# Performance work log

Measured on AMD Instinct MI355X. Metric: run time of the kernel, lower is better.

The kernel has to match this reference:

```python
import jax, jax.numpy as jnp
import numpy as np
import math

N, E, R = 50000, 800000, 32
DIN = 128
H, D = 8, 16          # num_heads, head_dim; H*D == out_ent_feats == 128
HOP = 5
ALPHA = 0.1
EPS = 1e-5


def layer_norm(x, g, b):
    m = jnp.mean(x, axis=-1, keepdims=True)
    v = jnp.mean((x - m) ** 2, axis=-1, keepdims=True)
    return (x - m) * jax.lax.rsqrt(v + EPS) * g + b


def segment_softmax(e, dst, num_nodes):
    # e: [E, H] scores, softmax over incoming edges of each dst node
    m = jax.ops.segment_max(e, dst, num_segments=num_nodes)      # [N, H]
    ex = jnp.exp(e - m[dst])
    s = jax.ops.segment_sum(ex, dst, num_segments=num_nodes)     # [N, H]
    return ex / s[dst]


def setup_inputs() -> dict:
    key = jax.random.key(0)
    ks = jax.random.split(key, 12)
    gain = 0.02  # small init scale (small_init_gain-style)
    ent_feat = jax.random.normal(ks[0], (N, DIN), dtype=jnp.float32)
    rel_feat = jax.random.normal(ks[1], (R, DIN), dtype=jnp.float32)
    src = jax.random.randint(ks[2], (E,), 0, N, dtype=jnp.int32)
    # guarantee every node has in-degree >= 1 (DGL raises otherwise)
    dst_rand = jax.random.randint(ks[3], (E - N,), 0, N, dtype=jnp.int32)
    dst = jnp.concatenate([jnp.arange(N, dtype=jnp.int32), dst_rand])
    rid = jax.random.randint(ks[4], (E,), 0, R, dtype=jnp.int32)
    W_head = jax.random.normal(ks[5], (DIN, H * D), dtype=jnp.float32) * gain
    W_tail = jax.random.normal(ks[6], (DIN, H * D), dtype=jnp.float32) * gain
    W_ent = jax.random.normal(ks[7], (DIN, H * D), dtype=jnp.float32) * gain
    W_rel = jax.random.normal(ks[8], (DIN, H * D), dtype=jnp.float32) * gain
    attn_r = jax.random.normal(ks[9], (1, H, D), dtype=jnp.float32) * gain
    W1 = jax.random.normal(ks[10], (H * D, 4 * H * D), dtype=jnp.float32) * gain
    W2 = jax.random.normal(ks[11], (4 * H * D, H * D), dtype=jnp.float32) * gain
    return dict(
        ent_feat=ent_feat, rel_feat=rel_feat, src=src, dst=dst, rid=rid,
        W_head=W_head, W_tail=W_tail, W_ent=W_ent, W_rel=W_rel, attn_r=attn_r,
        ln_ent_g=jnp.ones((DIN,), jnp.float32), ln_ent_b=jnp.zeros((DIN,), jnp.float32),
        ln_rel_g=jnp.ones((DIN,), jnp.float32), ln_rel_b=jnp.zeros((DIN,), jnp.float32),
        ff_ln_g=jnp.ones((H * D,), jnp.float32), ff_ln_b=jnp.zeros((H * D,), jnp.float32),
        W1=W1, b1=jnp.zeros((4 * H * D,), jnp.float32),
        W2=W2, b2=jnp.zeros((H * D,), jnp.float32),
    )


def _forward(ent_feat, rel_feat, src, dst, rid,
             W_head, W_tail, W_ent, W_rel, attn_r,
             ln_ent_g, ln_ent_b, ln_rel_g, ln_rel_b, ff_ln_g, ff_ln_b,
             W1, b1, W2, b2):
    n = ent_feat.shape[0]
    x = layer_norm(ent_feat, ln_ent_g, ln_ent_b)
    feat_head = (x @ W_head).reshape(n, H, D)
    feat_tail = (x @ W_tail).reshape(n, H, D)
    feat_ent = (x @ W_ent).reshape(n, H, D)

    # per-edge dot-product attention score: u_dot_v('eh','et')
    e = jnp.sum(feat_head[src] * feat_tail[dst], axis=-1)          # [E, H]

    r = layer_norm(rel_feat, ln_rel_g, ln_rel_b)
    feat_rel = (r @ W_rel).reshape(R, H, D)
    er = jnp.sum(feat_rel * attn_r, axis=-1)                       # [R, H]
    e = e * er[rid]                                                # [E, H]

    # e_mul_v with log_in = log(in_degree) of dst node
    deg = jax.ops.segment_sum(jnp.ones((e.shape[0],), e.dtype), dst, num_segments=n)
    log_in = jnp.log(jnp.maximum(deg, 1.0))                        # [N]
    e = e * log_in[dst][:, None] / math.sqrt(D)

    a = segment_softmax(e, dst, n)                                 # [E, H]

    # PPR diffusion: feat <- (1-alpha) * A^T feat + alpha * feat_0
    feat = feat_ent
    for _ in range(HOP):
        msg = feat[src] * a[:, :, None]                            # [E, H, D]
        agg = jax.ops.segment_sum(msg, dst, num_segments=n)        # [N, H, D]
        feat = (1.0 - ALPHA) * agg + ALPHA * feat_ent

    # residual (Identity: in_ent_feats == out_ent_feats)
    rst = feat + ent_feat.reshape(n, H, D)
    rst = rst.reshape(n, H * D)

    h = layer_norm(rst, ff_ln_g, ff_ln_b)
    ff = jax.nn.relu(h @ W1 + b1) @ W2 + b2
    return ff + rst


def reference(ent_feat, rel_feat, src, dst, rid,
              W_head, W_tail, W_ent, W_rel, attn_r,
              ln_ent_g, ln_ent_b, ln_rel_g, ln_rel_b, ff_ln_g, ff_ln_b,
              W1, b1, W2, b2):
    return _forward(ent_feat, rel_feat, src, dst, rid,
                    W_head, W_tail, W_ent, W_rel, attn_r,
                    ln_ent_g, ln_ent_b, ln_rel_g, ln_rel_b, ff_ln_g, ff_ln_b,
                    W1, b1, W2, b2)
```

## Files before the change

kernel.cpp:

```cpp
#include <hip/hip_runtime.h>
#include <hip/hip_bf16.h>

#define N_NODES 50000
#define N_EDGES 800000
#define N_REL 32
#define DIN 128
#define NH 8
#define HD 16
#define FF_HID 512
#define EPS_LN 1e-5f
#define NBUCK 8
#define BDIV 6250
#define BCAP 114688

typedef __attribute__((ext_vector_type(8))) short bf16x8;
typedef __attribute__((ext_vector_type(4))) float f32x4;
typedef __attribute__((ext_vector_type(2))) float f32x2;
typedef unsigned short ushort_t;
typedef unsigned int uint_t;

static __device__ __forceinline__ unsigned short f2bf(float f) {
    union { float f; unsigned u; } v; v.f = f;
    unsigned r = (v.u + 0x7fffu + ((v.u >> 16) & 1u)) >> 16;
    return (unsigned short)r;
}
static __device__ __forceinline__ float bf2f(unsigned u16) {
    union { unsigned u; float f; } v; v.u = u16 << 16; return v.f;
}
static __device__ __forceinline__ unsigned char f2fp8(float f) {
    return (unsigned char)(__builtin_amdgcn_cvt_pk_fp8_f32(f, f, 0, false) & 0xff);
}
static __device__ __forceinline__ uint_t f2fp8x2(float x0, float x1) {
    return (__builtin_amdgcn_cvt_pk_fp8_f32(x0, x1, 0, false) & 0xffffu);
}
static __device__ __forceinline__ void fp8x4_to_f32(uint_t w, float* o) {
    f32x2 lo = __builtin_amdgcn_cvt_pk_f32_fp8(w, false);
    f32x2 hi = __builtin_amdgcn_cvt_pk_f32_fp8(w, true);
    o[0] = lo.x; o[1] = lo.y; o[2] = hi.x; o[3] = hi.y;
}

static __device__ __forceinline__ void pack_dev(const float* __restrict__ W,
                                                short* __restrict__ out, int K, int Ncols,
                                                int idx) {
    int KT = K >> 5;
    int l = idx & 63;
    int tile = idx >> 6;
    int kt = tile & (KT - 1);
    int ct = tile / KT;
    int c = ct * 16 + (l & 15);
    int k0 = kt * 32 + ((l >> 4) * 8);
    bf16x8 v;
#pragma unroll
    for (int j = 0; j < 8; j++) v[j] = (short)f2bf(W[(size_t)(k0 + j) * Ncols + c]);
    *(bf16x8*)(out + (size_t)idx * 8) = v;
}

#define C0_BIN 512
__global__ __launch_bounds__(256) void combo0_kernel(
    const int* __restrict__ src, const int* __restrict__ dst, const int* __restrict__ rid,
    int* __restrict__ gcnt, int* __restrict__ bdst, int* __restrict__ bpay,
    const float* __restrict__ W1, short* __restrict__ W1p, const float* __restrict__ W2,
    short* __restrict__ W2p, const float* __restrict__ Wh, short* __restrict__ Whp,
    const float* __restrict__ Wt, short* __restrict__ Wtp, const float* __restrict__ We,
    short* __restrict__ Wep, const float* __restrict__ rel_feat,
    const float* __restrict__ gr, const float* __restrict__ br,
    const float* __restrict__ W_rel, const float* __restrict__ attn_r,
    float* __restrict__ er) {
    __shared__ float red[128];
    __shared__ float xsr[128];
    __shared__ float prod[128];
    __shared__ int cnt[NBUCK];
    __shared__ int sbase[NBUCK];
    int b = blockIdx.x, tid = threadIdx.x;
    if (b < C0_BIN) {
        const int chunk = (N_EDGES + C0_BIN - 1) / C0_BIN;
        int i0 = b * chunk;
        int i1 = min(i0 + chunk, N_EDGES);
        int rounds = (i1 - i0 + 255) >> 8;
        for (int r = 0; r < rounds; r++) {
            int i = i0 + (r << 8) + tid;
            if (tid < NBUCK) cnt[tid] = 0;
            __syncthreads();
            int d = 0, b8 = 0, rank = 0, py = 0;
            bool v = i < i1;
            if (v) {
                d = dst[i];
                b8 = d / BDIV;
                py = src[i] | (rid[i] << 16);
                rank = atomicAdd(&cnt[b8], 1);
            }
            __syncthreads();
            if (tid < NBUCK) sbase[tid] = atomicAdd(&gcnt[tid], cnt[tid]);
            __syncthreads();
            if (v) {
                size_t pos = (size_t)b8 * BCAP + sbase[b8] + rank;
                bdst[pos] = d;
                bpay[pos] = py;
            }
            __syncthreads();
        }
    } else if (b < C0_BIN + 32) {
        pack_dev(W1, W1p, DIN, FF_HID, (b - C0_BIN) * 256 + tid);
    } else if (b < C0_BIN + 64) {
        pack_dev(W2, W2p, FF_HID, DIN, (b - C0_BIN - 32) * 256 + tid);
    } else if (b < C0_BIN + 72) {
        pack_dev(Wh, Whp, DIN, DIN, (b - C0_BIN - 64) * 256 + tid);
    } else if (b < C0_BIN + 80) {
        pack_dev(Wt, Wtp, DIN, DIN, (b - C0_BIN - 72) * 256 + tid);
    } else if (b < C0_BIN + 88) {
        pack_dev(We, Wep, DIN, DIN, (b - C0_BIN - 80) * 256 + tid);
    } else {
        int r = b - (C0_BIN + 88);
        float x = 0.f;
        if (tid < 128) {
            x = rel_feat[r * DIN + tid];
            red[tid] = x;
        }
        __syncthreads();
        for (int off = 64; off > 0; off >>= 1) {
            if (tid < off) red[tid] += red[tid + off];
            __syncthreads();
        }
        float mean = red[0] * (1.f / DIN);
        __syncthreads();
        if (tid < 128) red[tid] = x * x;
        __syncthreads();
        for (int off = 64; off > 0; off >>= 1) {
            if (tid < off) red[tid] += red[tid + off];
            __syncthreads();
        }
        float var = red[0] * (1.f / DIN) - mean * mean;
        float rs = rsqrtf(var + EPS_LN);
        if (tid < 128) xsr[tid] = (x - mean) * rs * gr[tid] + br[tid];
        __syncthreads();
        if (tid < 128) {
            float acc = 0.f;
            for (int k = 0; k < DIN; k++) acc += xsr[k] * W_rel[k * DIN + tid];
            prod[tid] = acc * attn_r[tid];
        }
        __syncthreads();
        if (tid < NH) {
            float s = 0.f;
            for (int d = 0; d < HD; d++) s += prod[tid * HD + d];
            er[r * NH + tid] = s;
        }
    }
}

#define NHB 8
__global__ __launch_bounds__(256) void hist2_kernel(const int* __restrict__ bdst,
                                                    const int* __restrict__ gcnt,
                                                    int* __restrict__ deg) {
    __shared__ int lhist[BDIV];
    int blk = blockIdx.x, tid = threadIdx.x;
    int b8 = blk & 7, sub = blk >> 3;
    for (int i = tid; i < BDIV; i += 256) lhist[i] = 0;
    __syncthreads();
    int cnt = gcnt[b8];
    int chunk = (cnt + NHB - 1) / NHB;
    int i0 = sub * chunk;
    int i1 = min(i0 + chunk, cnt);
    const int* bp = bdst + (size_t)b8 * BCAP;
    int w0 = b8 * BDIV;
    for (int i = i0 + tid; i < i1; i += 256) atomicAdd(&lhist[bp[i] - w0], 1);
    __syncthreads();
    for (int i = tid; i < BDIV; i += 256) {
        int v = lhist[i];
        if (v) atomicAdd(&deg[w0 + i], v);
    }
}

#define NS_SCAN 196
__global__ __launch_bounds__(256) void combo_mid_kernel(
    const int* __restrict__ deg, int* __restrict__ row_off,
    const float* __restrict__ ent, const float* __restrict__ g, const float* __restrict__ b,
    const short* __restrict__ Whp, const short* __restrict__ Wtp,
    const short* __restrict__ Wep, unsigned char* __restrict__ hent,
    ushort_t* __restrict__ tail_bf) {
    __shared__ float xs[32][128];
    __shared__ short hsb[32][136];
    int blk = blockIdx.x, tid = threadIdx.x;
    if (blk < NS_SCAN) {
        __shared__ int lscan[256];
        __shared__ int ws4[4];
        int n = N_NODES;
        int start = blk * 256;
        int partial = 0;
        for (int i = tid; i < start; i += 256) partial += deg[i];
        for (int m = 32; m > 0; m >>= 1) partial += __shfl_down(partial, m);
        int wid = tid >> 6, lane = tid & 63;
        if (lane == 0) ws4[wid] = partial;
        __syncthreads();
        int sbase = ws4[0] + ws4[1] + ws4[2] + ws4[3];
        int i = start + tid;
        int v = (i < n) ? deg[i] : 0;
        lscan[tid] = v;
        __syncthreads();
        for (int off = 1; off < 256; off <<= 1) {
            int t = (tid >= off) ? lscan[tid - off] : 0;
            __syncthreads();
            lscan[tid] += t;
            __syncthreads();
        }
        if (i < n) row_off[i] = sbase + lscan[tid] - v;
        if (i == n - 1) row_off[n] = sbase + lscan[tid];
        return;
    }
    int base = (blk - NS_SCAN) * 32;
    {
        int c = tid & 127, rb = tid >> 7;
#pragma unroll
        for (int j = 0; j < 16; j++) {
            int r = j * 2 + rb;
            int row = base + r;
            xs[r][c] = (row < N_NODES) ? ent[(size_t)row * DIN + c] : 0.f;
        }
    }
    __syncthreads();
    int wave = tid >> 6, lane = tid & 63;
    {
        float g0 = g[lane], g1 = g[lane + 64], bb0 = b[lane], bb1 = b[lane + 64];
        for (int r = wave * 8; r < wave * 8 + 8; r++) {
            float x0 = xs[r][lane], x1 = xs[r][lane + 64];
            float s1 = x0 + x1, s2 = x0 * x0 + x1 * x1;
            for (int m = 1; m < 64; m <<= 1) {
                s1 += __shfl_xor(s1, m);
                s2 += __shfl_xor(s2, m);
            }
            float mean = s1 * (1.f / DIN);
            float var = s2 * (1.f / DIN) - mean * mean;
            float rs = rsqrtf(var + EPS_LN);
            hsb[r][lane] = (short)f2bf((x0 - mean) * rs * g0 + bb0);
            hsb[r][lane + 64] = (short)f2bf((x1 - mean) * rs * g1 + bb1);
        }
    }
    __syncthreads();
    bf16x8 a[2][4];
#pragma unroll
    for (int rt = 0; rt < 2; rt++)
#pragma unroll
        for (int kt = 0; kt < 4; kt++)
            a[rt][kt] = *(const bf16x8*)&hsb[rt * 16 + (lane & 15)][kt * 32 + (lane >> 4) * 8];
#pragma unroll
    for (int m = 0; m < 3; m++) {
        const bf16x8* bp = (m == 0)   ? (const bf16x8*)Whp
                           : (m == 1) ? (const bf16x8*)Wtp
                                      : (const bf16x8*)Wep;
#pragma unroll
        for (int c2 = 0; c2 < 2; c2++) {
            int ct = wave * 2 + c2;
            f32x4 acc0 = {0.f, 0.f, 0.f, 0.f}, acc1 = {0.f, 0.f, 0.f, 0.f};
#pragma unroll
            for (int kt = 0; kt < 4; kt++) {
                bf16x8 bf = bp[(ct * 4 + kt) * 64 + lane];
                acc0 = __builtin_amdgcn_mfma_f32_16x16x32_bf16(a[0][kt], bf, acc0, 0, 0, 0);
                acc1 = __builtin_amdgcn_mfma_f32_16x16x32_bf16(a[1][kt], bf, acc1, 0, 0, 0);
            }
            int col = ct * 16 + (lane & 15);
            int h = col >> 4, k = col & 15;
            int r0 = (lane >> 4) * 4;
#pragma unroll
            for (int j = 0; j < 4; j++) {
                int row0 = base + r0 + j, row1 = base + 16 + r0 + j;
                if (m == 0) {
                    if (row0 < N_NODES) hent[(size_t)row0 * 256 + h * 32 + k] = f2fp8(acc0[j]);
                    if (row1 < N_NODES) hent[(size_t)row1 * 256 + h * 32 + k] = f2fp8(acc1[j]);
                } else if (m == 1) {
                    if (row0 < N_NODES) tail_bf[(size_t)row0 * DIN + col] = f2bf(acc0[j]);
                    if (row1 < N_NODES) tail_bf[(size_t)row1 * DIN + col] = f2bf(acc1[j]);
                } else {
                    if (row0 < N_NODES)
                        hent[(size_t)row0 * 256 + h * 32 + 16 + k] = f2fp8(acc0[j]);
                    if (row1 < N_NODES)
                        hent[(size_t)row1 * 256 + h * 32 + 16 + k] = f2fp8(acc1[j]);
                }
            }
        }
    }
}

__global__ __launch_bounds__(256) void scatter_kernel(
    const int* __restrict__ bdst, const int* __restrict__ bpay,
    const int* __restrict__ gcnt, const int* __restrict__ row_off,
    int* __restrict__ cursor, int* __restrict__ sr_perm) {
    int blk = blockIdx.x, tid = threadIdx.x;
    int b8 = blk & 7, sub = blk >> 3;
    int cnt = gcnt[b8];
    int chunk = (cnt + 127) >> 7;
    int i0 = sub * chunk;
    int i1 = min(i0 + chunk, cnt);
    const int* bd = bdst + (size_t)b8 * BCAP;
    const int* bpp = bpay + (size_t)b8 * BCAP;
    for (int i = i0 + tid; i < i1; i += 256) {
        int d = bd[i];
        int p = row_off[d] + atomicAdd(&cursor[d], 1);
        sr_perm[p] = bpp[i];
    }
}

__global__ __launch_bounds__(256) void score_hop_kernel(
    const unsigned char* __restrict__ hent, const ushort_t* __restrict__ tail_bf,
    const float* __restrict__ er, const int* __restrict__ row_off,
    const int* __restrict__ sr_perm, ushort_t* __restrict__ a_bf,
    float* __restrict__ inv9, unsigned char* __restrict__ fout) {
    int wid = threadIdx.x >> 6;
    int u = blockIdx.x * 4 + wid;
    int lane = threadIdx.x & 63;
    int h = lane & 7, esub = lane >> 3;
    int p0 = row_off[u], p1 = row_off[u + 1];
    int deg = p1 - p0;
    float scale = logf((float)(deg > 0 ? deg : 1)) * 0.25f;
    float t[16];
    {
        const uint_t* tp = (const uint_t*)(tail_bf + (size_t)u * DIN + h * HD);
#pragma unroll
        for (int i = 0; i < 8; i++) {
            uint_t w = tp[i];
            t[2 * i] = bf2f(w & 0xffffu);
            t[2 * i + 1] = bf2f(w >> 16);
        }
    }
    float ssum = 0.f;
    float acc[16];
#pragma unroll
    for (int k = 0; k < 16; k++) acc[k] = 0.f;
    for (int p = p0 + esub; p < p1; p += 8) {
        int v = sr_perm[p];
        int s = v & 0xffff;
        int rr = v >> 16;
        const uint4* hp = (const uint4*)(hent + (size_t)s * 256 + h * 32);
        uint4 hw = hp[0];
        uint4 ew = hp[1];
        float hv[16], ev[16];
        fp8x4_to_f32(hw.x, hv + 0); fp8x4_to_f32(hw.y, hv + 4);
        fp8x4_to_f32(hw.z, hv + 8); fp8x4_to_f32(hw.w, hv + 12);
        fp8x4_to_f32(ew.x, ev + 0); fp8x4_to_f32(ew.y, ev + 4);
        fp8x4_to_f32(ew.z, ev + 8); fp8x4_to_f32(ew.w, ev + 12);
        float dot = 0.f;
#pragma unroll
        for (int k = 0; k < 16; k++) dot += t[k] * hv[k];
        float e = dot * er[rr * NH + h] * scale;
        float sx = expf(e);
        a_bf[(size_t)p * NH + h] = f2bf(sx);
        ssum += sx;
#pragma unroll
        for (int k = 0; k < 16; k++) acc[k] += sx * ev[k];
    }
    ssum += __shfl_xor(ssum, 8);
    ssum += __shfl_xor(ssum, 16);
    ssum += __shfl_xor(ssum, 32);
#pragma unroll
    for (int k = 0; k < 16; k++) {
        acc[k] += __shfl_xor(acc[k], 8);
        acc[k] += __shfl_xor(acc[k], 16);
        acc[k] += __shfl_xor(acc[k], 32);
    }
    if (esub == 0) {
        float iv = 0.9f / ssum;
        inv9[(size_t)u * NH + h] = iv;
        const uint4 eu = *(const uint4*)(hent + (size_t)u * 256 + h * 32 + 16);
        float e0[16];
        fp8x4_to_f32(eu.x, e0 + 0); fp8x4_to_f32(eu.y, e0 + 4);
        fp8x4_to_f32(eu.z, e0 + 8); fp8x4_to_f32(eu.w, e0 + 12);
        float x[16];
#pragma unroll
        for (int k = 0; k < 16; k++) x[k] = iv * acc[k] + 0.1f * e0[k];
        uint4 ov;
        ov.x = f2fp8x2(x[0], x[1]) | (f2fp8x2(x[2], x[3]) << 16);
        ov.y = f2fp8x2(x[4], x[5]) | (f2fp8x2(x[6], x[7]) << 16);
        ov.z = f2fp8x2(x[8], x[9]) | (f2fp8x2(x[10], x[11]) << 16);
        ov.w = f2fp8x2(x[12], x[13]) | (f2fp8x2(x[14], x[15]) << 16);
        *(uint4*)(fout + (size_t)u * DIN + h * HD) = ov;
    }
}

template <bool OUT_BF>
__global__ __launch_bounds__(256) void diffuse8_kernel(
    const unsigned char* __restrict__ fin8, const unsigned char* __restrict__ hent,
    const ushort_t* __restrict__ a_bf, const int* __restrict__ sr_perm,
    const int* __restrict__ row_off, const float* __restrict__ inv9,
    void* __restrict__ fout) {
    int wid = threadIdx.x >> 6;
    int u = blockIdx.x * 4 + wid;
    int lane = threadIdx.x & 63;
    int c = lane & 7;
    int g = lane >> 3;
    int p0 = row_off[u], p1 = row_off[u + 1];
    float acc[16];
#pragma unroll
    for (int j = 0; j < 16; j++) acc[j] = 0.f;
    for (int p = p0; p < p1; p += 8) {
        int pe = p + g;
        bool valid = pe < p1;
        int pc = valid ? pe : (p1 - 1);
        int s = sr_perm[pc] & 0xffff;
        float a = valid ? bf2f(a_bf[(size_t)pc * NH + c]) : 0.f;
        uint4 w = *(const uint4*)(fin8 + (size_t)s * DIN + 16 * c);
        float v[16];
        fp8x4_to_f32(w.x, v + 0);
        fp8x4_to_f32(w.y, v + 4);
        fp8x4_to_f32(w.z, v + 8);
        fp8x4_to_f32(w.w, v + 12);
#pragma unroll
        for (int j = 0; j < 16; j++) acc[j] += a * v[j];
    }
#pragma unroll
    for (int j = 0; j < 16; j++) {
        acc[j] += __shfl_xor(acc[j], 8);
        acc[j] += __shfl_xor(acc[j], 16);
        acc[j] += __shfl_xor(acc[j], 32);
    }
    if (g == 0) {
        float iv = inv9[(size_t)u * NH + c];
        uint4 ew = *(const uint4*)(hent + (size_t)u * 256 + c * 32 + 16);
        float e0[16];
        fp8x4_to_f32(ew.x, e0 + 0);
        fp8x4_to_f32(ew.y, e0 + 4);
        fp8x4_to_f32(ew.z, e0 + 8);
        fp8x4_to_f32(ew.w, e0 + 12);
        float x[16];
#pragma unroll
        for (int j = 0; j < 16; j++) x[j] = iv * acc[j] + 0.1f * e0[j];
        size_t o = (size_t)u * DIN + 16 * c;
        if (OUT_BF) {
            uint4 ov0, ov1;
            ov0.x = (uint_t)f2bf(x[0]) | ((uint_t)f2bf(x[1]) << 16);
            ov0.y = (uint_t)f2bf(x[2]) | ((uint_t)f2bf(x[3]) << 16);
            ov0.z = (uint_t)f2bf(x[4]) | ((uint_t)f2bf(x[5]) << 16);
            ov0.w = (uint_t)f2bf(x[6]) | ((uint_t)f2bf(x[7]) << 16);
            ov1.x = (uint_t)f2bf(x[8]) | ((uint_t)f2bf(x[9]) << 16);
            ov1.y = (uint_t)f2bf(x[10]) | ((uint_t)f2bf(x[11]) << 16);
            ov1.z = (uint_t)f2bf(x[12]) | ((uint_t)f2bf(x[13]) << 16);
            ov1.w = (uint_t)f2bf(x[14]) | ((uint_t)f2bf(x[15]) << 16);
            *(uint4*)((ushort_t*)fout + o) = ov0;
            *(uint4*)((ushort_t*)fout + o + 8) = ov1;
        } else {
            uint4 ov;
            ov.x = f2fp8x2(x[0], x[1]) | (f2fp8x2(x[2], x[3]) << 16);
            ov.y = f2fp8x2(x[4], x[5]) | (f2fp8x2(x[6], x[7]) << 16);
            ov.z = f2fp8x2(x[8], x[9]) | (f2fp8x2(x[10], x[11]) << 16);
            ov.w = f2fp8x2(x[12], x[13]) | (f2fp8x2(x[14], x[15]) << 16);
            *(uint4*)((unsigned char*)fout + o) = ov;
        }
    }
}

static __device__ __forceinline__ int hid_idx(int row, int col) {
    return row * 512 + ((((col >> 3) & 63) ^ (row & 7)) << 3) + (col & 7);
}
__global__ __launch_bounds__(256) void ffn_mfma_kernel(
    const ushort_t* __restrict__ feat, const float* __restrict__ ent0,
    const float* __restrict__ g, const float* __restrict__ b,
    const short* __restrict__ W1p, const float* __restrict__ b1,
    const short* __restrict__ W2p, const float* __restrict__ b2,
    float* __restrict__ out) {
    __shared__ ushort_t rst_bf[16][136];
    __shared__ short hs[16][136];
    __shared__ short hid[16 * 512];
    int tid = threadIdx.x;
    int base = blockIdx.x * 16;
    int wave = tid >> 6, lane = tid & 63;
    {
        int c = tid & 127, rb = tid >> 7;
#pragma unroll
        for (int j = 0; j < 8; j++) {
            int r = j * 2 + rb;
            int row = base + r;
            float v = 0.f;
            if (row < N_NODES) {
                size_t idx = (size_t)row * DIN + c;
                v = bf2f(feat[idx]) + ent0[idx];
            }
            rst_bf[r][c] = f2bf(v);
        }
    }
    __syncthreads();
    {
        float g0 = g[lane], g1 = g[lane + 64], bb0 = b[lane], bb1 = b[lane + 64];
        for (int r = wave * 4; r < wave * 4 + 4; r++) {
            float x0 = bf2f(rst_bf[r][lane]), x1 = bf2f(rst_bf[r][lane + 64]);
            float s1 = x0 + x1, s2 = x0 * x0 + x1 * x1;
            for (int m = 1; m < 64; m <<= 1) {
                s1 += __shfl_xor(s1, m);
                s2 += __shfl_xor(s2, m);
            }
            float mean = s1 * (1.f / DIN);
            float var = s2 * (1.f / DIN) - mean * mean;
            float rs = rsqrtf(var + EPS_LN);
            hs[r][lane] = (short)f2bf((x0 - mean) * rs * g0 + bb0);
            hs[r][lane + 64] = (short)f2bf((x1 - mean) * rs * g1 + bb1);
        }
    }
    __syncthreads();
    {
        bf16x8 a[4];
#pragma unroll
        for (int kt = 0; kt < 4; kt++)
            a[kt] = *(const bf16x8*)&hs[lane & 15][kt * 32 + (lane >> 4) * 8];
        const bf16x8* bp = (const bf16x8*)W1p;
        for (int cti = 0; cti < 8; cti++) {
            int ct = wave * 8 + cti;
            f32x4 acc0 = {0.f, 0.f, 0.f, 0.f};
#pragma unroll
            for (int kt = 0; kt < 4; kt++) {
                bf16x8 bf = bp[(ct * 4 + kt) * 64 + lane];
                acc0 = __builtin_amdgcn_mfma_f32_16x16x32_bf16(a[kt], bf, acc0, 0, 0, 0);
            }
            int col = ct * 16 + (lane & 15);
            float bv = b1[col];
            int r0 = (lane >> 4) * 4;
#pragma unroll
            for (int j = 0; j < 4; j++)
                hid[hid_idx(r0 + j, col)] = (short)f2bf(fmaxf(acc0[j] + bv, 0.f));
        }
    }
    __syncthreads();
    {
        f32x4 acc[2] = {{0.f, 0.f, 0.f, 0.f}, {0.f, 0.f, 0.f, 0.f}};
        const bf16x8* bp2 = (const bf16x8*)W2p;
        for (int kt = 0; kt < 16; kt++) {
            int col8 = kt * 32 + (lane >> 4) * 8;
            bf16x8 a0 = *(const bf16x8*)&hid[hid_idx(lane & 15, col8)];
#pragma unroll
            for (int c2 = 0; c2 < 2; c2++) {
                int ct = wave * 2 + c2;
                bf16x8 bf = bp2[(ct * 16 + kt) * 64 + lane];
                acc[c2] = __builtin_amdgcn_mfma_f32_16x16x32_bf16(a0, bf, acc[c2], 0, 0, 0);
            }
        }
#pragma unroll
        for (int c2 = 0; c2 < 2; c2++) {
            int col = (wave * 2 + c2) * 16 + (lane & 15);
            float bv = b2[col];
            int r0 = (lane >> 4) * 4;
#pragma unroll
            for (int j = 0; j < 4; j++) {
                int row = base + r0 + j;
                if (row < N_NODES)
                    out[(size_t)row * DIN + col] = acc[c2][j] + bv + bf2f(rst_bf[r0 + j][col]);
            }
        }
    }
}

extern "C" void kernel_launch(void* const* d_in, const int* in_sizes, int n_in,
                              void* d_out, int out_size, void* d_ws, size_t ws_size,
                              hipStream_t stream) {
    const float* ent_feat = (const float*)d_in[0];
    const float* rel_feat = (const float*)d_in[1];
    const int* src = (const int*)d_in[2];
    const int* dst = (const int*)d_in[3];
    const int* rid = (const int*)d_in[4];
    const float* W_head = (const float*)d_in[5];
    const float* W_tail = (const float*)d_in[6];
    const float* W_ent = (const float*)d_in[7];
    const float* W_rel = (const float*)d_in[8];
    const float* attn_r = (const float*)d_in[9];
    const float* ln_ent_g = (const float*)d_in[10];
    const float* ln_ent_b = (const float*)d_in[11];
    const float* ln_rel_g = (const float*)d_in[12];
    const float* ln_rel_b = (const float*)d_in[13];
    const float* ff_ln_g = (const float*)d_in[14];
    const float* ff_ln_b = (const float*)d_in[15];
    const float* W1 = (const float*)d_in[16];
    const float* b1 = (const float*)d_in[17];
    const float* W2 = (const float*)d_in[18];
    const float* b2 = (const float*)d_in[19];
    float* out = (float*)d_out;

    const int N = N_NODES, E = N_EDGES;

    char* cur = (char*)d_ws;
    auto alloc = [&](size_t bytes, size_t align) -> void* {
        uintptr_t p = (uintptr_t)cur;
        p = (p + align - 1) & ~(uintptr_t)(align - 1);
        cur = (char*)(p + bytes);
        return (void*)p;
    };
    ushort_t* tail_bf = (ushort_t*)alloc((size_t)N * DIN * 2, 16);
    unsigned char* hent = (unsigned char*)alloc((size_t)N * 256, 16);
    unsigned char* f8A = (unsigned char*)alloc((size_t)N * DIN, 16);
    unsigned char* f8B = (unsigned char*)alloc((size_t)N * DIN, 16);
    int* bdst = (int*)alloc((size_t)NBUCK * BCAP * 4, 16);
    int* bpay = (int*)alloc((size_t)NBUCK * BCAP * 4, 16);
    int* sr_perm = (int*)alloc((size_t)E * 4, 16);
    int* row_off = (int*)alloc((size_t)(N + 1) * 4, 16);
    int* deg = (int*)alloc(((size_t)2 * N + NBUCK) * 4, 16);
    int* cursor = deg + N;
    int* gcnt = deg + 2 * N;
    float* er = (float*)alloc((size_t)N_REL * NH * 4, 16);
    float* inv9 = (float*)alloc((size_t)N * NH * 4, 16);
    short* W1p = (short*)alloc((size_t)DIN * FF_HID * 2, 16);
    short* W2p = (short*)alloc((size_t)FF_HID * DIN * 2, 16);
    short* Whp = (short*)alloc((size_t)DIN * DIN * 2, 16);
    short* Wtp = (short*)alloc((size_t)DIN * DIN * 2, 16);
    short* Wep = (short*)alloc((size_t)DIN * DIN * 2, 16);
    ushort_t* a_fit = (ushort_t*)alloc((size_t)E * NH * 2, 16);
    bool a_in_ws = ((size_t)(cur - (char*)d_ws) <= ws_size);
    ushort_t* a_bf = a_in_ws ? a_fit : (ushort_t*)d_out;

    hipMemsetAsync(deg, 0, sizeof(int) * ((size_t)2 * N + NBUCK), stream);
    combo0_kernel<<<632, 256, 0, stream>>>(src, dst, rid, gcnt, bdst, bpay, W1, W1p, W2,
                                           W2p, W_head, Whp, W_tail, Wtp, W_ent, Wep,
                                           rel_feat, ln_rel_g, ln_rel_b, W_rel, attn_r,
                                           er);
    hist2_kernel<<<NBUCK * NHB, 256, 0, stream>>>(bdst, gcnt, deg);
    int nblk32 = (N + 31) / 32;
    combo_mid_kernel<<<NS_SCAN + nblk32, 256, 0, stream>>>(
        deg, row_off, ent_feat, ln_ent_g, ln_ent_b, Whp, Wtp, Wep, hent, tail_bf);
    scatter_kernel<<<1024, 256, 0, stream>>>(bdst, bpay, gcnt, row_off, cursor, sr_perm);
    score_hop_kernel<<<N / 4, 256, 0, stream>>>(hent, tail_bf, er, row_off, sr_perm,
                                                a_bf, inv9, f8A);
    diffuse8_kernel<false><<<N / 4, 256, 0, stream>>>(f8A, hent, a_bf, sr_perm, row_off,
                                                      inv9, f8B);
    diffuse8_kernel<false><<<N / 4, 256, 0, stream>>>(f8B, hent, a_bf, sr_perm, row_off,
                                                      inv9, f8A);
    diffuse8_kernel<false><<<N / 4, 256, 0, stream>>>(f8A, hent, a_bf, sr_perm, row_off,
                                                      inv9, f8B);
    diffuse8_kernel<true><<<N / 4, 256, 0, stream>>>(f8B, hent, a_bf, sr_perm, row_off,
                                                     inv9, tail_bf);
    int nblk16 = (N + 15) / 16;
    ffn_mfma_kernel<<<nblk16, 256, 0, stream>>>(tail_bf, ent_feat, ff_ln_g, ff_ln_b, W1p,
                                                b1, W2p, b2, out);
}
```

Before: 353.2 us.

## Fuse histogram with projection GEMM kernel and software-prefetch edge indices in gather loops

The degree histogram now runs in the same launch as the entity layernorm/projection blocks, and the prefix scan moves into its own small kernel. This overlaps histogram work with the GEMM instead of the scan overlapping with the GEMM. Separately, the score and diffusion loops load the next edge's index and attention weight one iteration ahead, so the dependent gather latency is partly hidden. The cost is a different kernel count and a bit more register pressure from the prefetch.

Result: slower. 362.2 us (+2.6%).

```diff
diff --git a/kernel.cpp b/kernel.cpp
--- a/kernel.cpp
+++ b/kernel.cpp
@@ -147,66 +147,38 @@
     }
 }
 
+#define C_HP_HIST 64
 #define NHB 8
-__global__ __launch_bounds__(256) void hist2_kernel(const int* __restrict__ bdst,
-                                                    const int* __restrict__ gcnt,
-                                                    int* __restrict__ deg) {
-    __shared__ int lhist[BDIV];
-    int blk = blockIdx.x, tid = threadIdx.x;
-    int b8 = blk & 7, sub = blk >> 3;
-    for (int i = tid; i < BDIV; i += 256) lhist[i] = 0;
-    __syncthreads();
-    int cnt = gcnt[b8];
-    int chunk = (cnt + NHB - 1) / NHB;
-    int i0 = sub * chunk;
-    int i1 = min(i0 + chunk, cnt);
-    const int* bp = bdst + (size_t)b8 * BCAP;
-    int w0 = b8 * BDIV;
-    for (int i = i0 + tid; i < i1; i += 256) atomicAdd(&lhist[bp[i] - w0], 1);
-    __syncthreads();
-    for (int i = tid; i < BDIV; i += 256) {
-        int v = lhist[i];
-        if (v) atomicAdd(&deg[w0 + i], v);
-    }
-}
-
-#define NS_SCAN 196
-__global__ __launch_bounds__(256) void combo_mid_kernel(
-    const int* __restrict__ deg, int* __restrict__ row_off,
+__global__ __launch_bounds__(256) void combo_hp_kernel(
+    const int* __restrict__ bdst, const int* __restrict__ gcnt, int* __restrict__ deg,
     const float* __restrict__ ent, const float* __restrict__ g, const float* __restrict__ b,
     const short* __restrict__ Whp, const short* __restrict__ Wtp,
     const short* __restrict__ Wep, unsigned char* __restrict__ hent,
     ushort_t* __restrict__ tail_bf) {
-    __shared__ float xs[32][128];
-    __shared__ short hsb[32][136];
+    __shared__ __align__(16) char smem[25088];
     int blk = blockIdx.x, tid = threadIdx.x;
-    if (blk < NS_SCAN) {
-        __shared__ int lscan[256];
-        __shared__ int ws4[4];
-        int n = N_NODES;
-        int start = blk * 256;
-        int partial = 0;
-        for (int i = tid; i < start; i += 256) partial += deg[i];
-        for (int m = 32; m > 0; m >>= 1) partial += __shfl_down(partial, m);
-        int wid = tid >> 6, lane = tid & 63;
-        if (lane == 0) ws4[wid] = partial;
-        __syncthreads();
-        int sbase = ws4[0] + ws4[1] + ws4[2] + ws4[3];
-        int i = start + tid;
-        int v = (i < n) ? deg[i] : 0;
-        lscan[tid] = v;
-        __syncthreads();
-        for (int off = 1; off < 256; off <<= 1) {
-            int t = (tid >= off) ? lscan[tid - off] : 0;
-            __syncthreads();
-            lscan[tid] += t;
-            __syncthreads();
-        }
-        if (i < n) row_off[i] = sbase + lscan[tid] - v;
-        if (i == n - 1) row_off[n] = sbase + lscan[tid];
+    if (blk < C_HP_HIST) {
+        int* lhist = (int*)smem;
+        int b8 = blk & 7, sub = blk >> 3;
+        for (int i = tid; i < BDIV; i += 256) lhist[i] = 0;
+        __syncthreads();
+        int cnt = gcnt[b8];
+        int chunk = (cnt + NHB - 1) / NHB;
+        int i0 = sub * chunk;
+        int i1 = min(i0 + chunk, cnt);
+        const int* bp = bdst + (size_t)b8 * BCAP;
+        int w0 = b8 * BDIV;
+        for (int i = i0 + tid; i < i1; i += 256) atomicAdd(&lhist[bp[i] - w0], 1);
+        __syncthreads();
+        for (int i = tid; i < BDIV; i += 256) {
+            int v = lhist[i];
+            if (v) atomicAdd(&deg[w0 + i], v);
+        }
         return;
     }
-    int base = (blk - NS_SCAN) * 32;
+    float (*xs)[128] = (float(*)[128])smem;
+    short (*hsb)[136] = (short(*)[136])(smem + 16384);
+    int base = (blk - C_HP_HIST) * 32;
     {
         int c = tid & 127, rb = tid >> 7;
 #pragma unroll
@@ -277,6 +249,33 @@
             }
         }
     }
+}
+
+__global__ __launch_bounds__(256) void scan2_kernel(const int* __restrict__ deg,
+                                                    int* __restrict__ row_off, int n) {
+    __shared__ int lscan[256];
+    __shared__ int ws4[4];
+    int blk = blockIdx.x, tid = threadIdx.x;
+    int start = blk * 256;
+    int partial = 0;
+    for (int i = tid; i < start; i += 256) partial += deg[i];
+    for (int m = 32; m > 0; m >>= 1) partial += __shfl_down(partial, m);
+    int wid = tid >> 6, lane = tid & 63;
+    if (lane == 0) ws4[wid] = partial;
+    __syncthreads();
+    int sbase = ws4[0] + ws4[1] + ws4[2] + ws4[3];
+    int i = start + tid;
+    int v = (i < n) ? deg[i] : 0;
+    lscan[tid] = v;
+    __syncthreads();
+    for (int off = 1; off < 256; off <<= 1) {
+        int t = (tid >= off) ? lscan[tid - off] : 0;
+        __syncthreads();
+        lscan[tid] += t;
+        __syncthreads();
+    }
+    if (i < n) row_off[i] = sbase + lscan[tid] - v;
+    if (i == n - 1) row_off[n] = sbase + lscan[tid];
 }
 
 __global__ __launch_bounds__(256) void scatter_kernel(
@@ -324,10 +323,13 @@
     float acc[16];
 #pragma unroll
     for (int k = 0; k < 16; k++) acc[k] = 0.f;
-    for (int p = p0 + esub; p < p1; p += 8) {
-        int v = sr_perm[p];
-        int s = v & 0xffff;
-        int rr = v >> 16;
+    int p = p0 + esub;
+    int vcur = (p < p1) ? sr_perm[p] : 0;
+    while (p < p1) {
+        int pn = p + 8;
+        int vnext = (pn < p1) ? sr_perm[pn] : 0;
+        int s = vcur & 0xffff;
+        int rr = vcur >> 16;
         const uint4* hp = (const uint4*)(hent + (size_t)s * 256 + h * 32);
         uint4 hw = hp[0];
         uint4 ew = hp[1];
@@ -345,6 +347,8 @@
         ssum += sx;
 #pragma unroll
         for (int k = 0; k < 16; k++) acc[k] += sx * ev[k];
+        vcur = vnext;
+        p = pn;
     }
     ssum += __shfl_xor(ssum, 8);
     ssum += __shfl_xor(ssum, 16);
@@ -389,20 +393,32 @@
     float acc[16];
 #pragma unroll
     for (int j = 0; j < 16; j++) acc[j] = 0.f;
-    for (int p = p0; p < p1; p += 8) {
-        int pe = p + g;
-        bool valid = pe < p1;
-        int pc = valid ? pe : (p1 - 1);
-        int s = sr_perm[pc] & 0xffff;
-        float a = valid ? bf2f(a_bf[(size_t)pc * NH + c]) : 0.f;
-        uint4 w = *(const uint4*)(fin8 + (size_t)s * DIN + 16 * c);
+    int p = p0;
+    int pc0 = min(p + g, p1 - 1);
+    bool val0 = (p + g) < p1;
+    int scur = sr_perm[pc0] & 0xffff;
+    float acur = val0 ? bf2f(a_bf[(size_t)pc0 * NH + c]) : 0.f;
+    while (p < p1) {
+        int pn = p + 8;
+        int snext = 0;
+        float anext = 0.f;
+        if (pn < p1) {
+            int pcn = min(pn + g, p1 - 1);
+            bool vn = (pn + g) < p1;
+            snext = sr_perm[pcn] & 0xffff;
+            anext = vn ? bf2f(a_bf[(size_t)pcn * NH + c]) : 0.f;
+        }
+        uint4 w = *(const uint4*)(fin8 + (size_t)scur * DIN + 16 * c);
         float v[16];
         fp8x4_to_f32(w.x, v + 0);
         fp8x4_to_f32(w.y, v + 4);
         fp8x4_to_f32(w.z, v + 8);
         fp8x4_to_f32(w.w, v + 12);
 #pragma unroll
-        for (int j = 0; j < 16; j++) acc[j] += a * v[j];
+        for (int j = 0; j < 16; j++) acc[j] += acur * v[j];
+        scur = snext;
+        acur = anext;
+        p = pn;
     }
 #pragma unroll
     for (int j = 0; j < 16; j++) {
@@ -604,10 +620,10 @@
                                            W2p, W_head, Whp, W_tail, Wtp, W_ent, Wep,
                                            rel_feat, ln_rel_g, ln_rel_b, W_rel, attn_r,
                                            er);
-    hist2_kernel<<<NBUCK * NHB, 256, 0, stream>>>(bdst, gcnt, deg);
     int nblk32 = (N + 31) / 32;
-    combo_mid_kernel<<<NS_SCAN + nblk32, 256, 0, stream>>>(
-        deg, row_off, ent_feat, ln_ent_g, ln_ent_b, Whp, Wtp, Wep, hent, tail_bf);
+    combo_hp_kernel<<<C_HP_HIST + nblk32, 256, 0, stream>>>(
+        bdst, gcnt, deg, ent_feat, ln_ent_g, ln_ent_b, Whp, Wtp, Wep, hent, tail_bf);
+    scan2_kernel<<<(N + 255) / 256, 256, 0, stream>>>(deg, row_off, N);
     scatter_kernel<<<1024, 256, 0, stream>>>(bdst, bpay, gcnt, row_off, cursor, sr_perm);
     score_hop_kernel<<<N / 4, 256, 0, stream>>>(hent, tail_bf, er, row_off, sr_perm,
                                                 a_bf, inv9, f8A);
```
